# Kernel optimization log

Measured on AMD Instinct MI355X. Metric: run time of the kernel, lower is better.

## Reference

```python
import jax, jax.numpy as jnp
import numpy as np

N, NFEAT, NHID, NH2, NCLASS = 16384, 512, 256, 64, 10


def setup_inputs() -> dict:
    key = jax.random.key(0)
    ks = jax.random.split(key, 12)
    x = jax.random.normal(ks[0], (N, NFEAT), dtype=jnp.float32)
    # dense (row-normalized-style) adjacency; sparsified to ~avg degree 32
    a = jax.random.uniform(ks[1], (N, N), dtype=jnp.float32)
    mask = (jax.random.uniform(ks[2], (N, N)) < (32.0 / N)).astype(jnp.float32)
    adj = a * mask / 32.0
    s = lambda fin: 1.0 / np.sqrt(fin)
    W1 = jax.random.uniform(ks[3], (NFEAT, NHID), jnp.float32, -s(NFEAT), s(NFEAT))
    b1 = jax.random.uniform(ks[4], (NHID,), jnp.float32, -s(NFEAT), s(NFEAT))
    W2 = jax.random.uniform(ks[5], (NHID, NH2), jnp.float32, -s(NHID), s(NHID))
    b2 = jax.random.uniform(ks[6], (NH2,), jnp.float32, -s(NHID), s(NHID))
    W3 = jax.random.uniform(ks[7], (NH2, 32), jnp.float32, -s(NH2), s(NH2))
    b3 = jax.random.uniform(ks[8], (32,), jnp.float32, -s(NH2), s(NH2))
    W4 = jax.random.uniform(ks[9], (32, 16), jnp.float32, -s(32), s(32))
    b4 = jax.random.uniform(ks[10], (16,), jnp.float32, -s(32), s(32))
    W5 = jax.random.uniform(ks[11], (16, NCLASS), jnp.float32, -s(16), s(16))
    b5 = jnp.zeros((NCLASS,), jnp.float32)
    return {"x": x, "adj": adj, "W1": W1, "b1": b1, "W2": W2, "b2": b2,
            "W3": W3, "b3": b3, "W4": W4, "b4": b4, "W5": W5, "b5": b5}


def reference(x, adj, W1, b1, W2, b2, W3, b3, W4, b4, W5, b5):
    # GraphConvolution: adj @ (x @ W) + b
    h = jax.nn.relu(adj @ (x @ W1) + b1)          # [N, NHID]
    h = adj @ (h @ W2) + b2                        # [N, 64]
    g = jnp.max(h, axis=0)                         # [64] graph max-pool
    g = jax.nn.relu(g @ W3 + b3)                   # [32]
    g = jax.nn.relu(g @ W4 + b4)                   # [16]
    return g @ W5 + b5                             # [NCLASS]
```

## Files before the change

### kernel.cpp

```cpp
#include <hip/hip_runtime.h>
#include <hip/hip_bf16.h>
#include <cstdint>

#define NROW 16384
#define NFEAT 512
#define NHID 256
#define NH2 64
#define CAP 96

typedef float vfloat4 __attribute__((ext_vector_type(4)));

#define BM 128
#define BN 64
#define BK 16

__global__ __launch_bounds__(256, 4) void kA_gemm(
    const float* __restrict__ X, const float* __restrict__ W1,
    float* __restrict__ XW1) {
  __shared__ float As[BK][BM + 4];
  __shared__ float Bs[BK][BN];
  const int t = threadIdx.x;
  const int bm = (blockIdx.x >> 2) * BM;
  const int bn = (blockIdx.x & 3) * BN;
  const int tx = t & 15;
  const int ty = t >> 4;
  const int ar = t >> 1;
  const int ak = (t & 1) * 8;
  const int bk = t >> 4;
  const int bnn = (t & 15) * 4;
  float acc[8][4] = {};
  for (int k0 = 0; k0 < NFEAT; k0 += BK) {
    const float4 a0 = *(const float4*)&X[(size_t)(bm + ar) * NFEAT + k0 + ak];
    const float4 a1 = *(const float4*)&X[(size_t)(bm + ar) * NFEAT + k0 + ak + 4];
    const float4 b0 = *(const float4*)&W1[(size_t)(k0 + bk) * NHID + bn + bnn];
    As[ak + 0][ar] = a0.x; As[ak + 1][ar] = a0.y;
    As[ak + 2][ar] = a0.z; As[ak + 3][ar] = a0.w;
    As[ak + 4][ar] = a1.x; As[ak + 5][ar] = a1.y;
    As[ak + 6][ar] = a1.z; As[ak + 7][ar] = a1.w;
    *(float4*)&Bs[bk][bnn] = b0;
    __syncthreads();
#pragma unroll
    for (int k = 0; k < BK; ++k) {
      float a[8], b[4];
#pragma unroll
      for (int i = 0; i < 8; ++i) a[i] = As[k][ty * 8 + i];
#pragma unroll
      for (int j = 0; j < 4; ++j) b[j] = Bs[k][tx * 4 + j];
#pragma unroll
      for (int i = 0; i < 8; ++i)
#pragma unroll
        for (int j = 0; j < 4; ++j) acc[i][j] += a[i] * b[j];
    }
    __syncthreads();
  }
#pragma unroll
  for (int i = 0; i < 8; ++i) {
    float4 v = {acc[i][0], acc[i][1], acc[i][2], acc[i][3]};
    *(float4*)&XW1[(size_t)(bm + ty * 8 + i) * NHID + bn + tx * 4] = v;
  }
}

__global__ __launch_bounds__(256, 6) void kB_stream_prop1(
    const float* __restrict__ adj, const float* __restrict__ XW1,
    const float* __restrict__ b1, const float* __restrict__ W2,
    float* __restrict__ vals, int* __restrict__ cols, int* __restrict__ cnt,
    float* __restrict__ H1W2) {
  __shared__ int   scl[4][CAP];
  __shared__ float sv[4][CAP];
  __shared__ float sh[4][NHID];
  __shared__ float sp[4][256];
  const int t = threadIdx.x;
  const int w = t >> 6, lane = t & 63;
  const int row0 = blockIdx.x * 4;
  const int row = row0 + w;

  const float* arow = adj + (size_t)row * NROW;
  int count = 0;

  auto process = [&](const vfloat4* buf, int base) {
#pragma unroll
    for (int j = 0; j < 4; ++j) {
      const vfloat4 v = buf[j];
      const unsigned long long anym =
          __ballot((v[0] != 0.0f) || (v[1] != 0.0f) ||
                   (v[2] != 0.0f) || (v[3] != 0.0f));
      if (anym == 0ull) continue;
#pragma unroll
      for (int k = 0; k < 4; ++k) {
        const float val = v[k];
        const unsigned long long m = __ballot(val != 0.0f);
        if (val != 0.0f) {
          const int pre = __builtin_amdgcn_mbcnt_hi(
              (uint32_t)(m >> 32), __builtin_amdgcn_mbcnt_lo((uint32_t)m, 0u));
          const int pos = count + pre;
          if (pos < CAP) { sv[w][pos] = val; scl[w][pos] = base + j * 256 + lane * 4 + k; }
        }
        count += (int)__popcll(m);
      }
    }
  };

  vfloat4 bufA[4], bufB[4];
#pragma unroll
  for (int j = 0; j < 4; ++j)
    bufA[j] = __builtin_nontemporal_load((const vfloat4*)&arow[j * 256 + lane * 4]);
  for (int c0 = 0; c0 < NROW; c0 += 2048) {
    if (c0 + 1024 < NROW) {
#pragma unroll
      for (int j = 0; j < 4; ++j)
        bufB[j] = __builtin_nontemporal_load(
            (const vfloat4*)&arow[c0 + 1024 + j * 256 + lane * 4]);
    }
    process(bufA, c0);
    if (c0 + 2048 < NROW) {
#pragma unroll
      for (int j = 0; j < 4; ++j)
        bufA[j] = __builtin_nontemporal_load(
            (const vfloat4*)&arow[c0 + 2048 + j * 256 + lane * 4]);
    }
    process(bufB, c0 + 1024);
  }

  const int n = count < CAP ? count : CAP;
  if (lane == 0) cnt[row] = n;
  for (int j = lane; j < n; j += 64) {
    cols[(size_t)row * CAP + j] = scl[w][j];
    vals[(size_t)row * CAP + j] = sv[w][j];
  }

  float4 a0 = {0,0,0,0}, a1 = {0,0,0,0}, a2 = {0,0,0,0}, a3 = {0,0,0,0};
  int k = 0;
  for (; k + 4 <= n; k += 4) {
    const float v0 = sv[w][k], v1 = sv[w][k+1], v2 = sv[w][k+2], v3 = sv[w][k+3];
    const int   c0i = scl[w][k], c1i = scl[w][k+1], c2i = scl[w][k+2], c3i = scl[w][k+3];
    const float4 x0 = *(const float4*)&XW1[(size_t)c0i * NHID + lane * 4];
    const float4 x1 = *(const float4*)&XW1[(size_t)c1i * NHID + lane * 4];
    const float4 x2 = *(const float4*)&XW1[(size_t)c2i * NHID + lane * 4];
    const float4 x3 = *(const float4*)&XW1[(size_t)c3i * NHID + lane * 4];
    a0.x += v0*x0.x; a0.y += v0*x0.y; a0.z += v0*x0.z; a0.w += v0*x0.w;
    a1.x += v1*x1.x; a1.y += v1*x1.y; a1.z += v1*x1.z; a1.w += v1*x1.w;
    a2.x += v2*x2.x; a2.y += v2*x2.y; a2.z += v2*x2.z; a2.w += v2*x2.w;
    a3.x += v3*x3.x; a3.y += v3*x3.y; a3.z += v3*x3.z; a3.w += v3*x3.w;
  }
  for (; k < n; ++k) {
    const float v0 = sv[w][k];
    const float4 x0 = *(const float4*)&XW1[(size_t)scl[w][k] * NHID + lane * 4];
    a0.x += v0*x0.x; a0.y += v0*x0.y; a0.z += v0*x0.z; a0.w += v0*x0.w;
  }
  const float4 bb = *(const float4*)&b1[lane * 4];
  float4 h;
  h.x = fmaxf(a0.x + a1.x + a2.x + a3.x + bb.x, 0.f);
  h.y = fmaxf(a0.y + a1.y + a2.y + a3.y + bb.y, 0.f);
  h.z = fmaxf(a0.z + a1.z + a2.z + a3.z + bb.z, 0.f);
  h.w = fmaxf(a0.w + a1.w + a2.w + a3.w + bb.w, 0.f);
  *(float4*)&sh[w][lane * 4] = h;
  __syncthreads();

  const int c = t & 63, q = t >> 6;
  float p0 = 0.f, p1 = 0.f, p2 = 0.f, p3 = 0.f;
#pragma unroll 8
  for (int kk = 0; kk < 64; ++kk) {
    const int kidx = q * 64 + kk;
    const float wv = W2[kidx * NH2 + c];
    p0 += sh[0][kidx] * wv;
    p1 += sh[1][kidx] * wv;
    p2 += sh[2][kidx] * wv;
    p3 += sh[3][kidx] * wv;
  }
  sp[0][t] = p0; sp[1][t] = p1; sp[2][t] = p2; sp[3][t] = p3;
  __syncthreads();
  {
    const int r2 = t >> 6, c2 = t & 63;
    H1W2[(size_t)(row0 + r2) * NH2 + c2] =
        sp[r2][c2] + sp[r2][c2 + 64] + sp[r2][c2 + 128] + sp[r2][c2 + 192];
  }
}

__global__ __launch_bounds__(256, 6) void kC_prop2(
    const float* __restrict__ H1W2, const float* __restrict__ vals,
    const int* __restrict__ cols, const int* __restrict__ cnt,
    const float* __restrict__ b2, float* __restrict__ blockmax) {
  __shared__ int   scl[4][CAP];
  __shared__ float sv[4][CAP];
  __shared__ float smax[4][NH2];
  const int t = threadIdx.x;
  const int w = t >> 6, l = t & 63;
  const int row = blockIdx.x * 4 + w;
  const int n = cnt[row];
  for (int jj = l; jj < n; jj += 64) {
    scl[w][jj] = cols[(size_t)row * CAP + jj];
    sv[w][jj]  = vals[(size_t)row * CAP + jj];
  }
  __syncthreads();
  float a0 = 0.f, a1 = 0.f, a2 = 0.f, a3 = 0.f;
  int k = 0;
  for (; k + 4 <= n; k += 4) {
    a0 += sv[w][k + 0] * H1W2[(size_t)scl[w][k + 0] * NH2 + l];
    a1 += sv[w][k + 1] * H1W2[(size_t)scl[w][k + 1] * NH2 + l];
    a2 += sv[w][k + 2] * H1W2[(size_t)scl[w][k + 2] * NH2 + l];
    a3 += sv[w][k + 3] * H1W2[(size_t)scl[w][k + 3] * NH2 + l];
  }
  for (; k < n; ++k) a0 += sv[w][k] * H1W2[(size_t)scl[w][k] * NH2 + l];
  smax[w][l] = a0 + a1 + a2 + a3 + b2[l];
  __syncthreads();
  if (t < NH2) {
    const float m = fmaxf(fmaxf(smax[0][t], smax[1][t]),
                          fmaxf(smax[2][t], smax[3][t]));
    blockmax[(size_t)blockIdx.x * NH2 + t] = m;
  }
}

__global__ __launch_bounds__(256) void kD1_colmax(const float* __restrict__ blockmax,
                                                  float* __restrict__ partial) {
  __shared__ float sm[256];
  const int t = threadIdx.x, c = t & 63, q = t >> 6;
  const int base = blockIdx.x * 64;
  float m = -3.4e38f;
  for (int r = q; r < 64; r += 4)
    m = fmaxf(m, blockmax[(size_t)(base + r) * NH2 + c]);
  sm[t] = m;
  __syncthreads();
  if (t < 64)
    partial[blockIdx.x * 64 + t] =
        fmaxf(fmaxf(sm[t], sm[t + 64]), fmaxf(sm[t + 128], sm[t + 192]));
}

__global__ __launch_bounds__(64) void kD2_final(const float* __restrict__ partial,
                                                const float* __restrict__ W3,
                                                const float* __restrict__ b3,
                                                const float* __restrict__ W4,
                                                const float* __restrict__ b4,
                                                const float* __restrict__ W5,
                                                const float* __restrict__ b5,
                                                float* __restrict__ out) {
  __shared__ float g[64], t3[32], t4[16];
  const int t = threadIdx.x;
  float m = -3.4e38f;
  for (int p = 0; p < 64; ++p) m = fmaxf(m, partial[p * 64 + t]);
  g[t] = m;
  __syncthreads();
  if (t < 32) {
    float acc = b3[t];
    for (int k = 0; k < 64; ++k) acc += g[k] * W3[k * 32 + t];
    t3[t] = acc > 0.f ? acc : 0.f;
  }
  __syncthreads();
  if (t < 16) {
    float acc = b4[t];
    for (int k = 0; k < 32; ++k) acc += t3[k] * W4[k * 16 + t];
    t4[t] = acc > 0.f ? acc : 0.f;
  }
  __syncthreads();
  if (t < 10) {
    float acc = b5[t];
    for (int k = 0; k < 16; ++k) acc += t4[k] * W5[k * 10 + t];
    out[t] = acc;
  }
}

extern "C" void kernel_launch(void* const* d_in, const int* in_sizes, int n_in,
                              void* d_out, int out_size, void* d_ws, size_t ws_size,
                              hipStream_t stream) {
  const float* x   = (const float*)d_in[0];
  const float* adj = (const float*)d_in[1];
  const float* W1  = (const float*)d_in[2];
  const float* b1  = (const float*)d_in[3];
  const float* W2  = (const float*)d_in[4];
  const float* b2  = (const float*)d_in[5];
  const float* W3  = (const float*)d_in[6];
  const float* b3  = (const float*)d_in[7];
  const float* W4  = (const float*)d_in[8];
  const float* b4  = (const float*)d_in[9];
  const float* W5  = (const float*)d_in[10];
  const float* b5  = (const float*)d_in[11];
  float* out = (float*)d_out;

  char* ws = (char*)d_ws;
  float* XW1      = (float*)(ws);
  float* vals     = (float*)(ws + (size_t)16 * 1024 * 1024);
  int*   cols     = (int*)  (ws + (size_t)24 * 1024 * 1024);
  int*   cnt      = (int*)  (ws + (size_t)32 * 1024 * 1024);
  float* H1W2     = (float*)(ws + (size_t)36 * 1024 * 1024);
  float* blockmax = (float*)(ws + (size_t)40 * 1024 * 1024);
  float* partial  = (float*)(ws + (size_t)44 * 1024 * 1024);

  kA_gemm<<<512, 256, 0, stream>>>(x, W1, XW1);
  kB_stream_prop1<<<NROW / 4, 256, 0, stream>>>(adj, XW1, b1, W2,
                                                vals, cols, cnt, H1W2);
  kC_prop2<<<NROW / 4, 256, 0, stream>>>(H1W2, vals, cols, cnt, b2, blockmax);
  kD1_colmax<<<64, 256, 0, stream>>>(blockmax, partial);
  kD2_final<<<1, 64, 0, stream>>>(partial, W3, b3, W4, b4, W5, b5, out);
}
```

Baseline: 1.449 ms.

## Fuse all GCN stages into one persistent kernel with atomic grid barriers

```diff
diff --git a/kernel.cpp b/kernel.cpp
--- a/kernel.cpp
+++ b/kernel.cpp
@@ -1,5 +1,4 @@
 #include <hip/hip_runtime.h>
-#include <hip/hip_bf16.h>
 #include <cstdint>
 
 #define NROW 16384
@@ -7,254 +6,277 @@
 #define NHID 256
 #define NH2 64
 #define CAP 96
+#define NBLK 1024u
 
 typedef float vfloat4 __attribute__((ext_vector_type(4)));
 
-#define BM 128
-#define BN 64
-#define BK 16
-
-__global__ __launch_bounds__(256, 4) void kA_gemm(
-    const float* __restrict__ X, const float* __restrict__ W1,
-    float* __restrict__ XW1) {
-  __shared__ float As[BK][BM + 4];
-  __shared__ float Bs[BK][BN];
+struct SmemA { float As[16][68]; float Bs[16][64]; };
+struct SmemB { int scl[4][CAP]; float sv[4][CAP]; float sh[4][NHID]; float sp[4][256]; };
+struct SmemC { int scl[4][CAP]; float sv[4][CAP]; float smax[4][NH2]; };
+struct SmemD { float sm[256]; };
+struct SmemE { float g[64]; float t3[32]; float t4[16]; };
+union Smem { SmemA a; SmemB b; SmemC c; SmemD d; SmemE e; };
+
+__device__ inline void grid_sync(unsigned* bar) {
+  __threadfence();
+  __syncthreads();
+  if (threadIdx.x == 0) {
+    const unsigned g =
+        __hip_atomic_load(&bar[1], __ATOMIC_ACQUIRE, __HIP_MEMORY_SCOPE_AGENT);
+    const unsigned a =
+        __hip_atomic_fetch_add(&bar[0], 1u, __ATOMIC_ACQ_REL, __HIP_MEMORY_SCOPE_AGENT);
+    if (a == NBLK - 1u) {
+      __hip_atomic_store(&bar[0], 0u, __ATOMIC_RELAXED, __HIP_MEMORY_SCOPE_AGENT);
+      __hip_atomic_fetch_add(&bar[1], 1u, __ATOMIC_RELEASE, __HIP_MEMORY_SCOPE_AGENT);
+    } else {
+      while (__hip_atomic_load(&bar[1], __ATOMIC_ACQUIRE, __HIP_MEMORY_SCOPE_AGENT) == g)
+        __builtin_amdgcn_s_sleep(1);
+    }
+  }
+  __syncthreads();
+  __threadfence();
+}
+
+__global__ __launch_bounds__(256, 4) void mega_gcn(
+    const float* __restrict__ X,   const float* __restrict__ W1,
+    const float* __restrict__ b1,  const float* __restrict__ W2,
+    const float* __restrict__ b2,  const float* __restrict__ W3,
+    const float* __restrict__ b3,  const float* __restrict__ W4,
+    const float* __restrict__ b4,  const float* __restrict__ W5,
+    const float* __restrict__ b5,  const float* __restrict__ adj,
+    float* __restrict__ XW1, float* __restrict__ vals, int* __restrict__ cols,
+    int* __restrict__ cnt, float* __restrict__ H1W2,
+    float* __restrict__ blockmax, float* __restrict__ partial,
+    float* __restrict__ out, unsigned* __restrict__ bar) {
+  __shared__ Smem smem;
   const int t = threadIdx.x;
-  const int bm = (blockIdx.x >> 2) * BM;
-  const int bn = (blockIdx.x & 3) * BN;
-  const int tx = t & 15;
-  const int ty = t >> 4;
-  const int ar = t >> 1;
-  const int ak = (t & 1) * 8;
-  const int bk = t >> 4;
-  const int bnn = (t & 15) * 4;
-  float acc[8][4] = {};
-  for (int k0 = 0; k0 < NFEAT; k0 += BK) {
-    const float4 a0 = *(const float4*)&X[(size_t)(bm + ar) * NFEAT + k0 + ak];
-    const float4 a1 = *(const float4*)&X[(size_t)(bm + ar) * NFEAT + k0 + ak + 4];
-    const float4 b0 = *(const float4*)&W1[(size_t)(k0 + bk) * NHID + bn + bnn];
-    As[ak + 0][ar] = a0.x; As[ak + 1][ar] = a0.y;
-    As[ak + 2][ar] = a0.z; As[ak + 3][ar] = a0.w;
-    As[ak + 4][ar] = a1.x; As[ak + 5][ar] = a1.y;
-    As[ak + 6][ar] = a1.z; As[ak + 7][ar] = a1.w;
-    *(float4*)&Bs[bk][bnn] = b0;
+  const int bid = blockIdx.x;
+
+  {
+    const int ty = t >> 4, tx = t & 15;
+    const int ar = t >> 2, ak = (t & 3) * 4;
+    const int bk = t >> 4, bn4 = (t & 15) * 4;
+    for (int tile = bid; tile < 1024; tile += (int)NBLK) {
+      const int bm = (tile >> 2) * 64;
+      const int bn = (tile & 3) * 64;
+      float acc[4][4] = {};
+      for (int k0 = 0; k0 < NFEAT; k0 += 16) {
+        const float4 av = *(const float4*)&X[(size_t)(bm + ar) * NFEAT + k0 + ak];
+        const float4 bv = *(const float4*)&W1[(size_t)(k0 + bk) * NHID + bn + bn4];
+        smem.a.As[ak + 0][ar] = av.x; smem.a.As[ak + 1][ar] = av.y;
+        smem.a.As[ak + 2][ar] = av.z; smem.a.As[ak + 3][ar] = av.w;
+        *(float4*)&smem.a.Bs[bk][bn4] = bv;
+        __syncthreads();
+#pragma unroll
+        for (int k = 0; k < 16; ++k) {
+          float a[4], b[4];
+#pragma unroll
+          for (int i = 0; i < 4; ++i) a[i] = smem.a.As[k][ty * 4 + i];
+#pragma unroll
+          for (int j = 0; j < 4; ++j) b[j] = smem.a.Bs[k][tx * 4 + j];
+#pragma unroll
+          for (int i = 0; i < 4; ++i)
+#pragma unroll
+            for (int j = 0; j < 4; ++j) acc[i][j] += a[i] * b[j];
+        }
+        __syncthreads();
+      }
+#pragma unroll
+      for (int i = 0; i < 4; ++i) {
+        float4 v = {acc[i][0], acc[i][1], acc[i][2], acc[i][3]};
+        *(float4*)&XW1[(size_t)(bm + ty * 4 + i) * NHID + bn + tx * 4] = v;
+      }
+    }
+  }
+  grid_sync(bar);
+
+  {
+    const int w = t >> 6, lane = t & 63;
+    for (int u = bid; u < NROW / 4; u += (int)NBLK) {
+      const int row0 = u * 4;
+      const int row = row0 + w;
+      const float* arow = adj + (size_t)row * NROW;
+      int count = 0;
+
+      auto process = [&](const vfloat4* buf, int base) {
+#pragma unroll
+        for (int j = 0; j < 4; ++j) {
+          const vfloat4 v = buf[j];
+          const unsigned long long anym =
+              __ballot((v[0] != 0.0f) || (v[1] != 0.0f) ||
+                       (v[2] != 0.0f) || (v[3] != 0.0f));
+          if (anym == 0ull) continue;
+#pragma unroll
+          for (int k = 0; k < 4; ++k) {
+            const float val = v[k];
+            const unsigned long long m = __ballot(val != 0.0f);
+            if (val != 0.0f) {
+              const int pre = __builtin_amdgcn_mbcnt_hi(
+                  (uint32_t)(m >> 32), __builtin_amdgcn_mbcnt_lo((uint32_t)m, 0u));
+              const int pos = count + pre;
+              if (pos < CAP) {
+                smem.b.sv[w][pos] = val;
+                smem.b.scl[w][pos] = base + j * 256 + lane * 4 + k;
+              }
+            }
+            count += (int)__popcll(m);
+          }
+        }
+      };
+
+      vfloat4 bufA[4], bufB[4];
+#pragma unroll
+      for (int j = 0; j < 4; ++j)
+        bufA[j] = __builtin_nontemporal_load((const vfloat4*)&arow[j * 256 + lane * 4]);
+      for (int c0 = 0; c0 < NROW; c0 += 2048) {
+        if (c0 + 1024 < NROW) {
+#pragma unroll
+          for (int j = 0; j < 4; ++j)
+            bufB[j] = __builtin_nontemporal_load(
+                (const vfloat4*)&arow[c0 + 1024 + j * 256 + lane * 4]);
+        }
+        process(bufA, c0);
+        if (c0 + 2048 < NROW) {
+#pragma unroll
+          for (int j = 0; j < 4; ++j)
+            bufA[j] = __builtin_nontemporal_load(
+                (const vfloat4*)&arow[c0 + 2048 + j * 256 + lane * 4]);
+        }
+        process(bufB, c0 + 1024);
+      }
+
+      const int n = count < CAP ? count : CAP;
+      if (lane == 0) cnt[row] = n;
+      for (int j = lane; j < n; j += 64) {
+        cols[(size_t)row * CAP + j] = smem.b.scl[w][j];
+        vals[(size_t)row * CAP + j] = smem.b.sv[w][j];
+      }
+
+      float4 a0 = {0,0,0,0}, a1 = {0,0,0,0}, a2 = {0,0,0,0}, a3 = {0,0,0,0};
+      int k = 0;
+      for (; k + 4 <= n; k += 4) {
+        const float v0 = smem.b.sv[w][k],   v1 = smem.b.sv[w][k+1];
+        const float v2 = smem.b.sv[w][k+2], v3 = smem.b.sv[w][k+3];
+        const int c0i = smem.b.scl[w][k],   c1i = smem.b.scl[w][k+1];
+        const int c2i = smem.b.scl[w][k+2], c3i = smem.b.scl[w][k+3];
+        const float4 x0 = *(const float4*)&XW1[(size_t)c0i * NHID + lane * 4];
+        const float4 x1 = *(const float4*)&XW1[(size_t)c1i * NHID + lane * 4];
+        const float4 x2 = *(const float4*)&XW1[(size_t)c2i * NHID + lane * 4];
+        const float4 x3 = *(const float4*)&XW1[(size_t)c3i * NHID + lane * 4];
+        a0.x += v0*x0.x; a0.y += v0*x0.y; a0.z += v0*x0.z; a0.w += v0*x0.w;
+        a1.x += v1*x1.x; a1.y += v1*x1.y; a1.z += v1*x1.z; a1.w += v1*x1.w;
+        a2.x += v2*x2.x; a2.y += v2*x2.y; a2.z += v2*x2.z; a2.w += v2*x2.w;
+        a3.x += v3*x3.x; a3.y += v3*x3.y; a3.z += v3*x3.z; a3.w += v3*x3.w;
+      }
+      for (; k < n; ++k) {
+        const float v0 = smem.b.sv[w][k];
+        const float4 x0 = *(const float4*)&XW1[(size_t)smem.b.scl[w][k] * NHID + lane * 4];
+        a0.x += v0*x0.x; a0.y += v0*x0.y; a0.z += v0*x0.z; a0.w += v0*x0.w;
+      }
+      const float4 bb = *(const float4*)&b1[lane * 4];
+      float4 h;
+      h.x = fmaxf(a0.x + a1.x + a2.x + a3.x + bb.x, 0.f);
+      h.y = fmaxf(a0.y + a1.y + a2.y + a3.y + bb.y, 0.f);
+      h.z = fmaxf(a0.z + a1.z + a2.z + a3.z + bb.z, 0.f);
+      h.w = fmaxf(a0.w + a1.w + a2.w + a3.w + bb.w, 0.f);
+      *(float4*)&smem.b.sh[w][lane * 4] = h;
+      __syncthreads();
+
+      const int c = t & 63, q = t >> 6;
+      float p0 = 0.f, p1 = 0.f, p2 = 0.f, p3 = 0.f;
+#pragma unroll 8
+      for (int kk = 0; kk < 64; ++kk) {
+        const int kidx = q * 64 + kk;
+        const float wv = W2[kidx * NH2 + c];
+        p0 += smem.b.sh[0][kidx] * wv;
+        p1 += smem.b.sh[1][kidx] * wv;
+        p2 += smem.b.sh[2][kidx] * wv;
+        p3 += smem.b.sh[3][kidx] * wv;
+      }
+      smem.b.sp[0][t] = p0; smem.b.sp[1][t] = p1;
+      smem.b.sp[2][t] = p2; smem.b.sp[3][t] = p3;
+      __syncthreads();
+      {
+        const int r2 = t >> 6, c2 = t & 63;
+        H1W2[(size_t)(row0 + r2) * NH2 + c2] =
+            smem.b.sp[r2][c2] + smem.b.sp[r2][c2 + 64] +
+            smem.b.sp[r2][c2 + 128] + smem.b.sp[r2][c2 + 192];
+      }
+      __syncthreads();
+    }
+  }
+  grid_sync(bar);
+
+  {
+    const int w = t >> 6, l = t & 63;
+    for (int u = bid; u < NROW / 4; u += (int)NBLK) {
+      const int row = u * 4 + w;
+      const int n = cnt[row];
+      for (int jj = l; jj < n; jj += 64) {
+        smem.c.scl[w][jj] = cols[(size_t)row * CAP + jj];
+        smem.c.sv[w][jj]  = vals[(size_t)row * CAP + jj];
+      }
+      __syncthreads();
+      float a0 = 0.f, a1 = 0.f, a2 = 0.f, a3 = 0.f;
+      int k = 0;
+      for (; k + 4 <= n; k += 4) {
+        a0 += smem.c.sv[w][k + 0] * H1W2[(size_t)smem.c.scl[w][k + 0] * NH2 + l];
+        a1 += smem.c.sv[w][k + 1] * H1W2[(size_t)smem.c.scl[w][k + 1] * NH2 + l];
+        a2 += smem.c.sv[w][k + 2] * H1W2[(size_t)smem.c.scl[w][k + 2] * NH2 + l];
+        a3 += smem.c.sv[w][k + 3] * H1W2[(size_t)smem.c.scl[w][k + 3] * NH2 + l];
+      }
+      for (; k < n; ++k) a0 += smem.c.sv[w][k] * H1W2[(size_t)smem.c.scl[w][k] * NH2 + l];
+      smem.c.smax[w][l] = a0 + a1 + a2 + a3 + b2[l];
+      __syncthreads();
+      if (t < NH2) {
+        const float m = fmaxf(fmaxf(smem.c.smax[0][t], smem.c.smax[1][t]),
+                              fmaxf(smem.c.smax[2][t], smem.c.smax[3][t]));
+        blockmax[(size_t)u * NH2 + t] = m;
+      }
+      __syncthreads();
+    }
+  }
+  grid_sync(bar);
+
+  if (bid < 64) {
+    const int c = t & 63, q = t >> 6;
+    const int base = bid * 64;
+    float m = -3.4e38f;
+    for (int r = q; r < 64; r += 4)
+      m = fmaxf(m, blockmax[(size_t)(base + r) * NH2 + c]);
+    smem.d.sm[t] = m;
     __syncthreads();
-#pragma unroll
-    for (int k = 0; k < BK; ++k) {
-      float a[8], b[4];
-#pragma unroll
-      for (int i = 0; i < 8; ++i) a[i] = As[k][ty * 8 + i];
-#pragma unroll
-      for (int j = 0; j < 4; ++j) b[j] = Bs[k][tx * 4 + j];
-#pragma unroll
-      for (int i = 0; i < 8; ++i)
-#pragma unroll
-        for (int j = 0; j < 4; ++j) acc[i][j] += a[i] * b[j];
+    if (t < 64)
+      partial[bid * 64 + t] =
+          fmaxf(fmaxf(smem.d.sm[t], smem.d.sm[t + 64]),
+                fmaxf(smem.d.sm[t + 128], smem.d.sm[t + 192]));
+  }
+  grid_sync(bar);
+
+  if (bid == 0) {
+    if (t < 64) {
+      float m = -3.4e38f;
+      for (int p = 0; p < 64; ++p) m = fmaxf(m, partial[p * 64 + t]);
+      smem.e.g[t] = m;
     }
     __syncthreads();
-  }
-#pragma unroll
-  for (int i = 0; i < 8; ++i) {
-    float4 v = {acc[i][0], acc[i][1], acc[i][2], acc[i][3]};
-    *(float4*)&XW1[(size_t)(bm + ty * 8 + i) * NHID + bn + tx * 4] = v;
-  }
-}
-
-__global__ __launch_bounds__(256, 6) void kB_stream_prop1(
-    const float* __restrict__ adj, const float* __restrict__ XW1,
-    const float* __restrict__ b1, const float* __restrict__ W2,
-    float* __restrict__ vals, int* __restrict__ cols, int* __restrict__ cnt,
-    float* __restrict__ H1W2) {
-  __shared__ int   scl[4][CAP];
-  __shared__ float sv[4][CAP];
-  __shared__ float sh[4][NHID];
-  __shared__ float sp[4][256];
-  const int t = threadIdx.x;
-  const int w = t >> 6, lane = t & 63;
-  const int row0 = blockIdx.x * 4;
-  const int row = row0 + w;
-
-  const float* arow = adj + (size_t)row * NROW;
-  int count = 0;
-
-  auto process = [&](const vfloat4* buf, int base) {
-#pragma unroll
-    for (int j = 0; j < 4; ++j) {
-      const vfloat4 v = buf[j];
-      const unsigned long long anym =
-          __ballot((v[0] != 0.0f) || (v[1] != 0.0f) ||
-                   (v[2] != 0.0f) || (v[3] != 0.0f));
-      if (anym == 0ull) continue;
-#pragma unroll
-      for (int k = 0; k < 4; ++k) {
-        const float val = v[k];
-        const unsigned long long m = __ballot(val != 0.0f);
-        if (val != 0.0f) {
-          const int pre = __builtin_amdgcn_mbcnt_hi(
-              (uint32_t)(m >> 32), __builtin_amdgcn_mbcnt_lo((uint32_t)m, 0u));
-          const int pos = count + pre;
-          if (pos < CAP) { sv[w][pos] = val; scl[w][pos] = base + j * 256 + lane * 4 + k; }
-        }
-        count += (int)__popcll(m);
-      }
-    }
-  };
-
-  vfloat4 bufA[4], bufB[4];
-#pragma unroll
-  for (int j = 0; j < 4; ++j)
-    bufA[j] = __builtin_nontemporal_load((const vfloat4*)&arow[j * 256 + lane * 4]);
-  for (int c0 = 0; c0 < NROW; c0 += 2048) {
-    if (c0 + 1024 < NROW) {
-#pragma unroll
-      for (int j = 0; j < 4; ++j)
-        bufB[j] = __builtin_nontemporal_load(
-            (const vfloat4*)&arow[c0 + 1024 + j * 256 + lane * 4]);
-    }
-    process(bufA, c0);
-    if (c0 + 2048 < NROW) {
-#pragma unroll
-      for (int j = 0; j < 4; ++j)
-        bufA[j] = __builtin_nontemporal_load(
-            (const vfloat4*)&arow[c0 + 2048 + j * 256 + lane * 4]);
-    }
-    process(bufB, c0 + 1024);
-  }
-
-  const int n = count < CAP ? count : CAP;
-  if (lane == 0) cnt[row] = n;
-  for (int j = lane; j < n; j += 64) {
-    cols[(size_t)row * CAP + j] = scl[w][j];
-    vals[(size_t)row * CAP + j] = sv[w][j];
-  }
-
-  float4 a0 = {0,0,0,0}, a1 = {0,0,0,0}, a2 = {0,0,0,0}, a3 = {0,0,0,0};
-  int k = 0;
-  for (; k + 4 <= n; k += 4) {
-    const float v0 = sv[w][k], v1 = sv[w][k+1], v2 = sv[w][k+2], v3 = sv[w][k+3];
-    const int   c0i = scl[w][k], c1i = scl[w][k+1], c2i = scl[w][k+2], c3i = scl[w][k+3];
-    const float4 x0 = *(const float4*)&XW1[(size_t)c0i * NHID + lane * 4];
-    const float4 x1 = *(const float4*)&XW1[(size_t)c1i * NHID + lane * 4];
-    const float4 x2 = *(const float4*)&XW1[(size_t)c2i * NHID + lane * 4];
-    const float4 x3 = *(const float4*)&XW1[(size_t)c3i * NHID + lane * 4];
-    a0.x += v0*x0.x; a0.y += v0*x0.y; a0.z += v0*x0.z; a0.w += v0*x0.w;
-    a1.x += v1*x1.x; a1.y += v1*x1.y; a1.z += v1*x1.z; a1.w += v1*x1.w;
-    a2.x += v2*x2.x; a2.y += v2*x2.y; a2.z += v2*x2.z; a2.w += v2*x2.w;
-    a3.x += v3*x3.x; a3.y += v3*x3.y; a3.z += v3*x3.z; a3.w += v3*x3.w;
-  }
-  for (; k < n; ++k) {
-    const float v0 = sv[w][k];
-    const float4 x0 = *(const float4*)&XW1[(size_t)scl[w][k] * NHID + lane * 4];
-    a0.x += v0*x0.x; a0.y += v0*x0.y; a0.z += v0*x0.z; a0.w += v0*x0.w;
-  }
-  const float4 bb = *(const float4*)&b1[lane * 4];
-  float4 h;
-  h.x = fmaxf(a0.x + a1.x + a2.x + a3.x + bb.x, 0.f);
-  h.y = fmaxf(a0.y + a1.y + a2.y + a3.y + bb.y, 0.f);
-  h.z = fmaxf(a0.z + a1.z + a2.z + a3.z + bb.z, 0.f);
-  h.w = fmaxf(a0.w + a1.w + a2.w + a3.w + bb.w, 0.f);
-  *(float4*)&sh[w][lane * 4] = h;
-  __syncthreads();
-
-  const int c = t & 63, q = t >> 6;
-  float p0 = 0.f, p1 = 0.f, p2 = 0.f, p3 = 0.f;
-#pragma unroll 8
-  for (int kk = 0; kk < 64; ++kk) {
-    const int kidx = q * 64 + kk;
-    const float wv = W2[kidx * NH2 + c];
-    p0 += sh[0][kidx] * wv;
-    p1 += sh[1][kidx] * wv;
-    p2 += sh[2][kidx] * wv;
-    p3 += sh[3][kidx] * wv;
-  }
-  sp[0][t] = p0; sp[1][t] = p1; sp[2][t] = p2; sp[3][t] = p3;
-  __syncthreads();
-  {
-    const int r2 = t >> 6, c2 = t & 63;
-    H1W2[(size_t)(row0 + r2) * NH2 + c2] =
-        sp[r2][c2] + sp[r2][c2 + 64] + sp[r2][c2 + 128] + sp[r2][c2 + 192];
-  }
-}
-
-__global__ __launch_bounds__(256, 6) void kC_prop2(
-    const float* __restrict__ H1W2, const float* __restrict__ vals,
-    const int* __restrict__ cols, const int* __restrict__ cnt,
-    const float* __restrict__ b2, float* __restrict__ blockmax) {
-  __shared__ int   scl[4][CAP];
-  __shared__ float sv[4][CAP];
-  __shared__ float smax[4][NH2];
-  const int t = threadIdx.x;
-  const int w = t >> 6, l = t & 63;
-  const int row = blockIdx.x * 4 + w;
-  const int n = cnt[row];
-  for (int jj = l; jj < n; jj += 64) {
-    scl[w][jj] = cols[(size_t)row * CAP + jj];
-    sv[w][jj]  = vals[(size_t)row * CAP + jj];
-  }
-  __syncthreads();
-  float a0 = 0.f, a1 = 0.f, a2 = 0.f, a3 = 0.f;
-  int k = 0;
-  for (; k + 4 <= n; k += 4) {
-    a0 += sv[w][k + 0] * H1W2[(size_t)scl[w][k + 0] * NH2 + l];
-    a1 += sv[w][k + 1] * H1W2[(size_t)scl[w][k + 1] * NH2 + l];
-    a2 += sv[w][k + 2] * H1W2[(size_t)scl[w][k + 2] * NH2 + l];
-    a3 += sv[w][k + 3] * H1W2[(size_t)scl[w][k + 3] * NH2 + l];
-  }
-  for (; k < n; ++k) a0 += sv[w][k] * H1W2[(size_t)scl[w][k] * NH2 + l];
-  smax[w][l] = a0 + a1 + a2 + a3 + b2[l];
-  __syncthreads();
-  if (t < NH2) {
-    const float m = fmaxf(fmaxf(smax[0][t], smax[1][t]),
-                          fmaxf(smax[2][t], smax[3][t]));
-    blockmax[(size_t)blockIdx.x * NH2 + t] = m;
-  }
-}
-
-__global__ __launch_bounds__(256) void kD1_colmax(const float* __restrict__ blockmax,
-                                                  float* __restrict__ partial) {
-  __shared__ float sm[256];
-  const int t = threadIdx.x, c = t & 63, q = t >> 6;
-  const int base = blockIdx.x * 64;
-  float m = -3.4e38f;
-  for (int r = q; r < 64; r += 4)
-    m = fmaxf(m, blockmax[(size_t)(base + r) * NH2 + c]);
-  sm[t] = m;
-  __syncthreads();
-  if (t < 64)
-    partial[blockIdx.x * 64 + t] =
-        fmaxf(fmaxf(sm[t], sm[t + 64]), fmaxf(sm[t + 128], sm[t + 192]));
-}
-
-__global__ __launch_bounds__(64) void kD2_final(const float* __restrict__ partial,
-                                                const float* __restrict__ W3,
-                                                const float* __restrict__ b3,
-                                                const float* __restrict__ W4,
-                                                const float* __restrict__ b4,
-                                                const float* __restrict__ W5,
-                                                const float* __restrict__ b5,
-                                                float* __restrict__ out) {
-  __shared__ float g[64], t3[32], t4[16];
-  const int t = threadIdx.x;
-  float m = -3.4e38f;
-  for (int p = 0; p < 64; ++p) m = fmaxf(m, partial[p * 64 + t]);
-  g[t] = m;
-  __syncthreads();
-  if (t < 32) {
-    float acc = b3[t];
-    for (int k = 0; k < 64; ++k) acc += g[k] * W3[k * 32 + t];
-    t3[t] = acc > 0.f ? acc : 0.f;
-  }
-  __syncthreads();
-  if (t < 16) {
-    float acc = b4[t];
-    for (int k = 0; k < 32; ++k) acc += t3[k] * W4[k * 16 + t];
-    t4[t] = acc > 0.f ? acc : 0.f;
-  }
-  __syncthreads();
-  if (t < 10) {
-    float acc = b5[t];
-    for (int k = 0; k < 16; ++k) acc += t4[k] * W5[k * 10 + t];
-    out[t] = acc;
+    if (t < 32) {
+      float acc = b3[t];
+      for (int k = 0; k < 64; ++k) acc += smem.e.g[k] * W3[k * 32 + t];
+      smem.e.t3[t] = acc > 0.f ? acc : 0.f;
+    }
+    __syncthreads();
+    if (t < 16) {
+      float acc = b4[t];
+      for (int k = 0; k < 32; ++k) acc += smem.e.t3[k] * W4[k * 16 + t];
+      smem.e.t4[t] = acc > 0.f ? acc : 0.f;
+    }
+    __syncthreads();
+    if (t < 10) {
+      float acc = b5[t];
+      for (int k = 0; k < 16; ++k) acc += smem.e.t4[k] * W5[k * 10 + t];
+      out[t] = acc;
+    }
   }
 }
 
@@ -283,11 +305,10 @@
   float* H1W2     = (float*)(ws + (size_t)36 * 1024 * 1024);
   float* blockmax = (float*)(ws + (size_t)40 * 1024 * 1024);
   float* partial  = (float*)(ws + (size_t)44 * 1024 * 1024);
-
-  kA_gemm<<<512, 256, 0, stream>>>(x, W1, XW1);
-  kB_stream_prop1<<<NROW / 4, 256, 0, stream>>>(adj, XW1, b1, W2,
-                                                vals, cols, cnt, H1W2);
-  kC_prop2<<<NROW / 4, 256, 0, stream>>>(H1W2, vals, cols, cnt, b2, blockmax);
-  kD1_colmax<<<64, 256, 0, stream>>>(blockmax, partial);
-  kD2_final<<<1, 64, 0, stream>>>(partial, W3, b3, W4, b4, W5, b5, out);
+  unsigned* bar   = (unsigned*)(ws + (size_t)45 * 1024 * 1024);
+
+  hipMemsetAsync(bar, 0, 16, stream);
+  mega_gcn<<<dim3(NBLK), dim3(256), 0, stream>>>(
+      x, W1, b1, W2, b2, W3, b3, W4, b4, W5, b5, adj,
+      XW1, vals, cols, cnt, H1W2, blockmax, partial, out, bar);
 }
```

Result: slower. 2.857 ms (+97.2%).
